# Kernel tuning notes

Hardware: AMD Instinct MI355X
Metric: run time of the kernel (lower is better)

Reference implementation:

```python
import jax, jax.numpy as jnp
import numpy as np

STRIDES = (4, 8, 16, 32, 64)
SIZES = (32.0, 64.0, 128.0, 256.0, 512.0)
ASPECT_RATIOS = np.array([0.5, 1.0, 2.0], dtype=np.float32)
IMG_H = IMG_W = 1024.0
PRE_NMS_TOPK = 1000   # per level (test)
POST_NMS_TOPK = 1000  # per image (test)
NMS_THRESH = 0.7
SCALE_CLAMP = float(np.log(1000.0 / 16.0))
LVL_OFFSET = 4096.0   # > max image coord, for batched (per-level) NMS


def _conv(x, w, b, pad):
    y = jax.lax.conv_general_dilated(x, w, (1, 1), pad,
                                     dimension_numbers=('NCHW', 'OIHW', 'NCHW'))
    return y + b[None, :, None, None]


def _level_anchors(H, W, stride, size):
    # cell anchors: area = size^2, h/w = aspect_ratio
    ar = jnp.asarray(ASPECT_RATIOS)
    w = size / jnp.sqrt(ar)
    h = w * ar
    base = jnp.stack([-w / 2, -h / 2, w / 2, h / 2], axis=1)  # [A,4]
    sx = (jnp.arange(W) * stride).astype(jnp.float32)
    sy = (jnp.arange(H) * stride).astype(jnp.float32)
    yy, xx = jnp.meshgrid(sy, sx, indexing='ij')
    shifts = jnp.stack([xx, yy, xx, yy], axis=-1).reshape(-1, 1, 4)  # [HW,1,4]
    return (shifts + base[None]).reshape(-1, 4)  # [H*W*A, 4]


def _decode_and_clip(deltas, anchors):
    wa = anchors[..., 2] - anchors[..., 0]
    ha = anchors[..., 3] - anchors[..., 1]
    cxa = anchors[..., 0] + 0.5 * wa
    cya = anchors[..., 1] + 0.5 * ha
    dx, dy = deltas[..., 0], deltas[..., 1]
    dw = jnp.minimum(deltas[..., 2], SCALE_CLAMP)
    dh = jnp.minimum(deltas[..., 3], SCALE_CLAMP)
    cx = dx * wa + cxa
    cy = dy * ha + cya
    w = jnp.exp(dw) * wa
    h = jnp.exp(dh) * ha
    x1 = jnp.clip(cx - 0.5 * w, 0.0, IMG_W)
    y1 = jnp.clip(cy - 0.5 * h, 0.0, IMG_H)
    x2 = jnp.clip(cx + 0.5 * w, 0.0, IMG_W)
    y2 = jnp.clip(cy + 0.5 * h, 0.0, IMG_H)
    return jnp.stack([x1, y1, x2, y2], axis=-1)


def _nms_single(raw_boxes, off_boxes, scores):
    # greedy NMS on (level-offset) boxes; returns POST_NMS_TOPK boxes + scores
    N = scores.shape[0]
    order = jnp.argsort(-scores)
    b = jax.lax.stop_gradient(off_boxes[order])
    rb = raw_boxes[order]
    s = scores[order]
    areas = (b[:, 2] - b[:, 0]) * (b[:, 3] - b[:, 1])
    idxs = jnp.arange(N)

    def body(i, sup):
        lt = jnp.maximum(b[i, :2], b[:, :2])
        rbr = jnp.minimum(b[i, 2:], b[:, 2:])
        wh = jnp.clip(rbr - lt, 0.0)
        inter = wh[:, 0] * wh[:, 1]
        iou = inter / (areas[i] + areas - inter + 1e-9)
        return sup | ((~sup[i]) & (iou > NMS_THRESH) & (idxs > i))

    sup = jax.lax.fori_loop(0, N, body, jnp.zeros((N,), bool))
    masked = jnp.where(sup, -1e9, s)
    top_s, top_i = jax.lax.top_k(masked, POST_NMS_TOPK)
    return rb[top_i], top_s


def _rpn_forward(feats, conv_w, conv_b, obj_w, obj_b, delta_w, delta_b):
    all_boxes, all_off, all_scores = [], [], []
    for lvl, (x, stride, size) in enumerate(zip(feats, STRIDES, SIZES)):
        t = jax.nn.relu(_conv(x, conv_w, conv_b, ((1, 1), (1, 1))))
        obj = _conv(t, obj_w, obj_b, ((0, 0), (0, 0)))        # [B,A,H,W]
        dlt = _conv(t, delta_w, delta_b, ((0, 0), (0, 0)))    # [B,4A,H,W]
        B, A, H, W = obj.shape
        obj = obj.transpose(0, 2, 3, 1).reshape(B, -1)        # [B, H*W*A]
        dlt = dlt.reshape(B, A, 4, H, W).transpose(0, 3, 4, 1, 2).reshape(B, -1, 4)
        anchors = _level_anchors(H, W, stride, size)          # [H*W*A, 4]
        k = min(PRE_NMS_TOPK, H * W * A)
        scores_k, idx = jax.lax.top_k(obj, k)                 # [B,k]
        deltas_k = jnp.take_along_axis(dlt, idx[..., None], axis=1)
        anchors_k = anchors[idx]                              # [B,k,4]
        boxes = _decode_and_clip(deltas_k, anchors_k)         # [B,k,4]
        all_boxes.append(boxes)
        all_off.append(boxes + lvl * LVL_OFFSET)              # per-level NMS trick
        all_scores.append(scores_k)
    boxes = jnp.concatenate(all_boxes, axis=1)    # [B, M, 4]
    off = jnp.concatenate(all_off, axis=1)        # [B, M, 4]
    scores = jnp.concatenate(all_scores, axis=1)  # [B, M]
    prop, sc = jax.vmap(_nms_single)(boxes, off, scores)  # [B,K,4], [B,K]
    return jnp.concatenate([prop, sc[..., None]], axis=-1)  # [B,K,5]


def setup_inputs() -> dict:
    key = jax.random.key(0)
    ks = jax.random.split(key, 10)
    C = 256
    shapes = [(2, C, 256, 256), (2, C, 128, 128), (2, C, 64, 64), (2, C, 32, 32), (2, C, 16, 16)]
    inp = {}
    for i, sh in enumerate(shapes):
        inp[f'feat{i}'] = jax.random.normal(ks[i], sh, dtype=jnp.float32)
    inp['conv_w'] = jax.random.normal(ks[5], (C, C, 3, 3), dtype=jnp.float32) * 0.02
    inp['conv_b'] = jnp.zeros((C,), jnp.float32)
    inp['obj_w'] = jax.random.normal(ks[6], (3, C, 1, 1), dtype=jnp.float32) * 0.02
    inp['obj_b'] = jnp.zeros((3,), jnp.float32)
    inp['delta_w'] = jax.random.normal(ks[7], (12, C, 1, 1), dtype=jnp.float32) * 0.02
    inp['delta_b'] = jnp.zeros((12,), jnp.float32)
    return inp


def reference(feat0, feat1, feat2, feat3, feat4, conv_w, conv_b, obj_w, obj_b, delta_w, delta_b):
    feats = [feat0, feat1, feat2, feat3, feat4]
    return _rpn_forward(feats, conv_w, conv_b, obj_w, obj_b, delta_w, delta_b)
```

## Files before the change

kernel.cpp:

```cpp
#include <hip/hip_runtime.h>
#include <cstdint>

#define PIX_TOTAL 87296
#define ATOT      261888
#define PS        2618880
#define MTOT      4768
#define SCALE_CLAMP 4.135166556742356f
#define WSTR      65

__device__ __forceinline__ unsigned fmono(float f) {
  unsigned u = __float_as_uint(f);
  return (u & 0x80000000u) ? ~u : (u | 0x80000000u);
}
__device__ __forceinline__ int lvl_pxb(int l) {
  switch (l) { case 0: return 0; case 1: return 65536; case 2: return 81920;
               case 3: return 86016; default: return 87040; }
}

template<int TW, int TH, int PXT>
__global__ void __launch_bounds__(512, 4)
conv3_fused(const float* __restrict__ feat, const float* __restrict__ cw,
            const float* __restrict__ cbias, const float* __restrict__ ow,
            const float* __restrict__ dw, float* __restrict__ partial,
            int H, int W, int px_base)
{
  constexpr int SR    = TW + 4;
  constexpr int ROWSZ = (TH + 2) * SR;
  constexpr int IN_N  = 8 * ROWSZ;
  constexpr int NR    = PXT / 4 + 1;

  const int tid  = threadIdx.x;
  const int tc   = tid & 7;
  const int tp   = tid >> 3;
  const int cblk = blockIdx.y;
  const int img  = blockIdx.z;
  const int tilesx = W / TW;
  const int ty = blockIdx.x / tilesx;
  const int tx = blockIdx.x - ty * tilesx;
  const int y0 = ty * TH, x0 = tx * TW;
  const int p  = tp * PXT;
  const int py = p / TW, px = p % TW;

  __shared__ __align__(16) float in_lds[IN_N];
  __shared__ __align__(16) float w_lds[8 * 9 * WSTR];
  __shared__ __align__(16) float wo_lds[15 * 64];

  for (int l = tid; l < 960; l += 512) {
    int o = l >> 6, c = l & 63;
    int cg = cblk * 64 + c;
    wo_lds[l] = (o < 3) ? ow[o * 256 + cg] : dw[(o - 3) * 256 + cg];
  }

  float acc[PXT][8];
  #pragma unroll
  for (int j = 0; j < PXT; ++j)
    #pragma unroll
    for (int c = 0; c < 8; ++c) acc[j][c] = 0.f;

  const float* fbase = feat + (size_t)img * 256 * H * W;

  for (int c0 = 0; c0 < 256; c0 += 8) {
    __syncthreads();
    for (int l = tid; l < IN_N; l += 512) {
      int ci  = l / ROWSZ;
      int rem = l - ci * ROWSZ;
      int yy  = rem / SR, xx = rem - yy * SR;
      int gy = y0 - 1 + yy, gx = x0 - 1 + xx;
      float v = 0.f;
      if (gy >= 0 && gy < H && gx >= 0 && gx < W)
        v = fbase[((c0 + ci) * H + gy) * W + gx];
      in_lds[l] = v;
    }
    {
      int oc = tid >> 3, ci = tid & 7;
      const float* wp = cw + ((size_t)(cblk * 64 + oc) * 256 + (c0 + ci)) * 9;
      #pragma unroll
      for (int tap = 0; tap < 9; ++tap)
        w_lds[(ci * 9 + tap) * WSTR + oc] = wp[tap];
    }
    __syncthreads();
    for (int ci = 0; ci < 8; ++ci) {
      #pragma unroll
      for (int ky = 0; ky < 3; ++ky) {
        const float* row = &in_lds[(ci * (TH + 2) + py + ky) * SR + px];
        float win[4 * NR];
        #pragma unroll
        for (int rr = 0; rr < NR; ++rr) {
          float4 rv = *(const float4*)(row + 4 * rr);
          win[4*rr+0] = rv.x; win[4*rr+1] = rv.y;
          win[4*rr+2] = rv.z; win[4*rr+3] = rv.w;
        }
        #pragma unroll
        for (int kx = 0; kx < 3; ++kx) {
          const float* wb = &w_lds[(ci * 9 + ky * 3 + kx) * WSTR + tc * 8];
          float4 w0 = *(const float4*)wb;
          float4 w1 = *(const float4*)(wb + 4);
          #pragma unroll
          for (int j = 0; j < PXT; ++j) {
            float bv = win[j + kx];
            acc[j][0] = fmaf(bv, w0.x, acc[j][0]);
            acc[j][1] = fmaf(bv, w0.y, acc[j][1]);
            acc[j][2] = fmaf(bv, w0.z, acc[j][2]);
            acc[j][3] = fmaf(bv, w0.w, acc[j][3]);
            acc[j][4] = fmaf(bv, w1.x, acc[j][4]);
            acc[j][5] = fmaf(bv, w1.y, acc[j][5]);
            acc[j][6] = fmaf(bv, w1.z, acc[j][6]);
            acc[j][7] = fmaf(bv, w1.w, acc[j][7]);
          }
        }
      }
    }
  }

  float tv[PXT][8];
  #pragma unroll
  for (int c = 0; c < 8; ++c) {
    float b = cbias[cblk * 64 + tc * 8 + c];
    #pragma unroll
    for (int j = 0; j < PXT; ++j) tv[j][c] = fmaxf(acc[j][c] + b, 0.f);
  }
  const int gy = y0 + py;
  const int gx0 = x0 + px;
  const size_t pbase = (size_t)cblk * PS +
      ((size_t)img * PIX_TOTAL + px_base + gy * W + gx0) * 15;
  for (int o = 0; o < 15; ++o) {
    const float* wb = &wo_lds[o * 64 + tc * 8];
    float4 w0 = *(const float4*)wb;
    float4 w1 = *(const float4*)(wb + 4);
    float s[PXT];
    #pragma unroll
    for (int j = 0; j < PXT; ++j)
      s[j] = tv[j][0]*w0.x + tv[j][1]*w0.y + tv[j][2]*w0.z + tv[j][3]*w0.w
           + tv[j][4]*w1.x + tv[j][5]*w1.y + tv[j][6]*w1.z + tv[j][7]*w1.w;
    #pragma unroll
    for (int m = 1; m < 8; m <<= 1) {
      #pragma unroll
      for (int j = 0; j < PXT; ++j) s[j] += __shfl_xor(s[j], m, 64);
    }
    if (tc == 0) {
      #pragma unroll
      for (int j = 0; j < PXT; ++j)
        partial[pbase + (size_t)j * 15 + o] = s[j];
    }
  }
}

__global__ void __launch_bounds__(256)
reduce_kernel(const float* __restrict__ partial, const float* __restrict__ ob,
              const float* __restrict__ db, float* __restrict__ scores,
              float* __restrict__ deltas)
{
  int v = blockIdx.x * 256 + threadIdx.x;
  if (v >= PS) return;
  float s = ((partial[v] + partial[(size_t)PS + v]) + partial[(size_t)2 * PS + v])
            + partial[(size_t)3 * PS + v];
  int o = v % 15;
  int pv = v / 15;
  if (o < 3) {
    scores[(size_t)pv * 3 + o] = s + ob[o];
  } else {
    int c = o - 3;
    deltas[((size_t)pv * 3 + (c >> 2)) * 4 + (c & 3)] = s + db[c];
  }
}

__global__ void __launch_bounds__(1024)
topk_kernel(const float* __restrict__ scores, float* __restrict__ sel_s,
            unsigned* __restrict__ sel_i)
{
  const int tid = threadIdx.x;
  const int bid = blockIdx.x;
  const int img = bid / 5, lvl = bid % 5;
  const int W = 256 >> lvl;
  const int N = W * W * 3;
  const int k = N < 1000 ? N : 1000;
  const float* sc = scores + (size_t)img * ATOT + (size_t)lvl_pxb(lvl) * 3;

  __shared__ unsigned hist[256];
  __shared__ unsigned sh_pref, sh_want;
  __shared__ int cnt_gt, cnt_tie;
  __shared__ float ss[1024];
  __shared__ unsigned si[1024];
  __shared__ unsigned ties[2048];

  unsigned prefix = 0; unsigned want = (unsigned)k;
  for (int pass = 0; pass < 4; ++pass) {
    const int shift = 24 - 8 * pass;
    if (tid < 256) hist[tid] = 0;
    __syncthreads();
    for (int i = tid; i < N; i += 1024) {
      unsigned u = fmono(sc[i]);
      if (pass == 0 || (u >> (shift + 8)) == prefix)
        atomicAdd(&hist[(u >> shift) & 255u], 1u);
    }
    __syncthreads();
    if (tid == 0) {
      unsigned cum = 0; int b = 255;
      for (; b > 0; --b) {
        if (cum + hist[b] >= want) break;
        cum += hist[b];
      }
      sh_pref = (prefix << 8) | (unsigned)b;
      sh_want = want - cum;
    }
    __syncthreads();
    prefix = sh_pref; want = sh_want;
    __syncthreads();
  }
  const unsigned T = prefix;

  ss[tid] = -3e38f; si[tid] = 0xFFFFFFFFu;
  if (tid == 0) { cnt_gt = 0; cnt_tie = 0; }
  __syncthreads();
  for (int i = tid; i < N; i += 1024) {
    float f = sc[i];
    unsigned u = fmono(f);
    if (u > T) {
      int pos = atomicAdd(&cnt_gt, 1);
      ss[pos] = f; si[pos] = (unsigned)i;
    } else if (u == T) {
      int pos = atomicAdd(&cnt_tie, 1);
      if (pos < 2048) ties[pos] = (unsigned)i;
    }
  }
  __syncthreads();
  const int cg = cnt_gt;
  int need = k - cg;
  const int tn = cnt_tie < 2048 ? cnt_tie : 2048;
  if (need > tn) need = tn;
  for (int e = tid; e < tn; e += 1024) {
    unsigned mye = ties[e];
    int rank = 0;
    for (int j = 0; j < tn; ++j) rank += (ties[j] < mye) ? 1 : 0;
    if (rank < need) { ss[cg + rank] = sc[mye]; si[cg + rank] = mye; }
  }
  __syncthreads();
  for (int k2 = 2; k2 <= 1024; k2 <<= 1) {
    for (int j2 = k2 >> 1; j2 > 0; j2 >>= 1) {
      int l2 = tid ^ j2;
      if (l2 > tid) {
        float a = ss[tid], b = ss[l2];
        unsigned ia = si[tid], ib = si[l2];
        bool less = (a < b) || (a == b && ia > ib);
        bool up = ((tid & k2) == 0);
        if (less == up) { ss[tid] = b; ss[l2] = a; si[tid] = ib; si[l2] = ia; }
      }
      __syncthreads();
    }
  }
  sel_s[(size_t)bid * 1024 + tid] = ss[tid];
  sel_i[(size_t)bid * 1024 + tid] = si[tid];
}

__global__ void __launch_bounds__(256)
decode_kernel(const unsigned* __restrict__ sel_i, const float* __restrict__ deltas,
              float* __restrict__ braw, float* __restrict__ boff)
{
  int g = blockIdx.x * 256 + threadIdx.x;
  if (g >= 10240) return;
  int bid = g >> 10, r = g & 1023;
  int img = bid / 5, lvl = bid % 5;
  int W = 256 >> lvl, N = W * W * 3;
  int k = N < 1000 ? N : 1000;
  if (r >= k) return;
  unsigned idx = sel_i[(size_t)bid * 1024 + r];
  float obx[4] = {0.f, 0.f, 0.f, 0.f};
  if (idx < (unsigned)N) {
    int a = idx % 3;
    int pix = idx / 3;
    int x = pix % W, y = pix / W;
    float ar = (a == 0) ? 0.5f : (a == 1 ? 1.0f : 2.0f);
    float sz = (float)(32 << lvl);
    float stridef = (float)(4 << lvl);
    float wa0 = __fdiv_rn(sz, __fsqrt_rn(ar));
    float ha0 = __fmul_rn(wa0, ar);
    float sx = __fmul_rn((float)x, stridef);
    float sy = __fmul_rn((float)y, stridef);
    float x1a = __fadd_rn(sx, -0.5f * wa0);
    float y1a = __fadd_rn(sy, -0.5f * ha0);
    float x2a = __fadd_rn(sx,  0.5f * wa0);
    float y2a = __fadd_rn(sy,  0.5f * ha0);
    float wa  = __fsub_rn(x2a, x1a);
    float ha  = __fsub_rn(y2a, y1a);
    float cxa = __fadd_rn(x1a, __fmul_rn(0.5f, wa));
    float cya = __fadd_rn(y1a, __fmul_rn(0.5f, ha));
    const float* dl = deltas + ((size_t)img * ATOT + (size_t)lvl_pxb(lvl) * 3 + idx) * 4;
    float dx = dl[0], dy = dl[1];
    float dwv = fminf(dl[2], SCALE_CLAMP);
    float dhv = fminf(dl[3], SCALE_CLAMP);
    float cx = __fadd_rn(__fmul_rn(dx, wa), cxa);
    float cy = __fadd_rn(__fmul_rn(dy, ha), cya);
    float wb = __fmul_rn(expf(dwv), wa);
    float hb = __fmul_rn(expf(dhv), ha);
    obx[0] = fminf(fmaxf(__fsub_rn(cx, __fmul_rn(0.5f, wb)), 0.f), 1024.f);
    obx[1] = fminf(fmaxf(__fsub_rn(cy, __fmul_rn(0.5f, hb)), 0.f), 1024.f);
    obx[2] = fminf(fmaxf(__fadd_rn(cx, __fmul_rn(0.5f, wb)), 0.f), 1024.f);
    obx[3] = fminf(fmaxf(__fadd_rn(cy, __fmul_rn(0.5f, hb)), 0.f), 1024.f);
  }
  float loff = (float)lvl * 4096.0f;
  size_t o = ((size_t)bid * 1024 + r) * 4;
  braw[o + 0] = obx[0]; braw[o + 1] = obx[1];
  braw[o + 2] = obx[2]; braw[o + 3] = obx[3];
  boff[o + 0] = __fadd_rn(obx[0], loff); boff[o + 1] = __fadd_rn(obx[1], loff);
  boff[o + 2] = __fadd_rn(obx[2], loff); boff[o + 3] = __fadd_rn(obx[3], loff);
}

__global__ void __launch_bounds__(256)
nms_kernel(const float* __restrict__ boff, unsigned* __restrict__ sup_out)
{
  const int bid = blockIdx.x;
  const int lvl = bid % 5;
  const int W = 256 >> lvl;
  const int N = W * W * 3;
  const int k = N < 1000 ? N : 1000;
  const int tid = threadIdx.x;
  __shared__ float bx1[1000], by1[1000], bx2[1000], by2[1000], bar_[1000];
  __shared__ int sup[1000];
  for (int i = tid; i < k; i += 256) {
    const float* b = boff + ((size_t)bid * 1024 + i) * 4;
    float x1 = b[0], y1 = b[1], x2 = b[2], y2 = b[3];
    bx1[i] = x1; by1[i] = y1; bx2[i] = x2; by2[i] = y2;
    bar_[i] = __fmul_rn(__fsub_rn(x2, x1), __fsub_rn(y2, y1));
    sup[i] = 0;
  }
  __syncthreads();
  for (int i = 0; i < k - 1; ++i) {
    if (!sup[i]) {
      float xi1 = bx1[i], yi1 = by1[i], xi2 = bx2[i], yi2 = by2[i], ai = bar_[i];
      for (int j = i + 1 + tid; j < k; j += 256) {
        if (sup[j]) continue;
        float lx = fmaxf(xi1, bx1[j]);
        float ly = fmaxf(yi1, by1[j]);
        float rx = fminf(xi2, bx2[j]);
        float ry = fminf(yi2, by2[j]);
        float w2 = fmaxf(__fsub_rn(rx, lx), 0.f);
        float h2 = fmaxf(__fsub_rn(ry, ly), 0.f);
        float inter = __fmul_rn(w2, h2);
        float den = __fadd_rn(__fsub_rn(__fadd_rn(ai, bar_[j]), inter), 1e-9f);
        if (__fdiv_rn(inter, den) > 0.7f) sup[j] = 1;
      }
    }
    __syncthreads();
  }
  for (int i = tid; i < k; i += 256) sup_out[(size_t)bid * 1024 + i] = (unsigned)sup[i];
}

__global__ void __launch_bounds__(1024)
merge_kernel(const float* __restrict__ sel_s, const unsigned* __restrict__ sup,
             const float* __restrict__ braw, float* __restrict__ out)
{
  const int img = blockIdx.x;
  const int tid = threadIdx.x;
  __shared__ float ms[MTOT];
  for (int e = tid; e < MTOT; e += 1024) {
    int lvl = e < 4000 ? e / 1000 : 4;
    int r = e - lvl * 1000;
    size_t p2 = (size_t)(img * 5 + lvl) * 1024 + r;
    ms[e] = sup[p2] ? -1e9f : sel_s[p2];
  }
  __syncthreads();
  for (int e = tid; e < MTOT; e += 1024) {
    float me = ms[e];
    int rank = 0;
    for (int j = 0; j < MTOT; ++j) {
      float mj = ms[j];
      rank += (mj > me || (mj == me && j < e)) ? 1 : 0;
    }
    if (rank < 1000) {
      int lvl = e < 4000 ? e / 1000 : 4;
      int r = e - lvl * 1000;
      const float* b = braw + ((size_t)(img * 5 + lvl) * 1024 + r) * 4;
      float* o = out + ((size_t)img * 1000 + rank) * 5;
      o[0] = b[0]; o[1] = b[1]; o[2] = b[2]; o[3] = b[3]; o[4] = me;
    }
  }
}

extern "C" void kernel_launch(void* const* d_in, const int* in_sizes, int n_in,
                              void* d_out, int out_size, void* d_ws, size_t ws_size,
                              hipStream_t stream)
{
  const float* f0 = (const float*)d_in[0];
  const float* f1 = (const float*)d_in[1];
  const float* f2 = (const float*)d_in[2];
  const float* f3 = (const float*)d_in[3];
  const float* f4 = (const float*)d_in[4];
  const float* cw = (const float*)d_in[5];
  const float* cb = (const float*)d_in[6];
  const float* ow = (const float*)d_in[7];
  const float* ob = (const float*)d_in[8];
  const float* dw = (const float*)d_in[9];
  const float* db = (const float*)d_in[10];
  float* out = (float*)d_out;

  float* ws       = (float*)d_ws;
  float* partial  = ws;
  float* scores   = ws + (size_t)4 * PS;
  float* deltas   = scores + (size_t)2 * ATOT;
  float* sel_s    = deltas + (size_t)8 * ATOT;
  unsigned* sel_i = (unsigned*)(sel_s + 10240);
  float* braw     = (float*)(sel_i + 10240);
  float* boff     = braw + 40960;
  unsigned* sup   = (unsigned*)(boff + 40960);

  conv3_fused<128, 4, 8><<<dim3(128, 4, 2), 512, 0, stream>>>(f0, cw, cb, ow, dw, partial, 256, 256, 0);
  conv3_fused<128, 4, 8><<<dim3( 32, 4, 2), 512, 0, stream>>>(f1, cw, cb, ow, dw, partial, 128, 128, 65536);
  conv3_fused< 64, 8, 8><<<dim3(  8, 4, 2), 512, 0, stream>>>(f2, cw, cb, ow, dw, partial,  64,  64, 81920);
  conv3_fused< 32,16, 8><<<dim3(  2, 4, 2), 512, 0, stream>>>(f3, cw, cb, ow, dw, partial,  32,  32, 86016);
  conv3_fused< 16,16, 4><<<dim3(  1, 4, 2), 512, 0, stream>>>(f4, cw, cb, ow, dw, partial,  16,  16, 87040);
  reduce_kernel<<<PS / 256, 256, 0, stream>>>(partial, ob, db, scores, deltas);
  topk_kernel<<<10, 1024, 0, stream>>>(scores, sel_s, sel_i);
  decode_kernel<<<40, 256, 0, stream>>>(sel_i, deltas, braw, boff);
  nms_kernel<<<10, 256, 0, stream>>>(boff, sup);
  merge_kernel<<<2, 1024, 0, stream>>>(sel_s, sup, braw, out);
}
```

Baseline: 9.503 ms.

## Replace serial NMS with bitmask IoU matrix and single-wave suppression scan

Replaces the per-level greedy NMS, which ran one block-wide barrier per candidate box, with two phases. First all pairwise IoU tests are computed in parallel into 64-bit suppression masks held in shared memory. Then a single wavefront scans the rows sequentially using shuffles and no block barriers. It also drops the minBlocks=4 occupancy hint on the conv kernel's launch bounds, which relaxes the register cap. The cost is about 128KB of shared memory for the masks, and every pair is now computed even when the box is already suppressed.

```diff
diff --git a/kernel.cpp b/kernel.cpp
--- a/kernel.cpp
+++ b/kernel.cpp
@@ -7,6 +7,7 @@
 #define MTOT      4768
 #define SCALE_CLAMP 4.135166556742356f
 #define WSTR      65
+#define NW        16
 
 __device__ __forceinline__ unsigned fmono(float f) {
   unsigned u = __float_as_uint(f);
@@ -18,7 +19,7 @@
 }
 
 template<int TW, int TH, int PXT>
-__global__ void __launch_bounds__(512, 4)
+__global__ void __launch_bounds__(512)
 conv3_fused(const float* __restrict__ feat, const float* __restrict__ cw,
             const float* __restrict__ cbias, const float* __restrict__ ow,
             const float* __restrict__ dw, float* __restrict__ partial,
@@ -305,8 +306,9 @@
   boff[o + 2] = __fadd_rn(obx[2], loff); boff[o + 3] = __fadd_rn(obx[3], loff);
 }
 
-__global__ void __launch_bounds__(256)
-nms_kernel(const float* __restrict__ boff, unsigned* __restrict__ sup_out)
+#define BBI(j) ((j) + ((j) >> 6))
+__global__ void __launch_bounds__(1024)
+nms_fused(const float* __restrict__ boff, unsigned* __restrict__ sup_out)
 {
   const int bid = blockIdx.x;
   const int lvl = bid % 5;
@@ -314,35 +316,67 @@
   const int N = W * W * 3;
   const int k = N < 1000 ? N : 1000;
   const int tid = threadIdx.x;
-  __shared__ float bx1[1000], by1[1000], bx2[1000], by2[1000], bar_[1000];
-  __shared__ int sup[1000];
-  for (int i = tid; i < k; i += 256) {
+
+  __shared__ __align__(16) float4 bb[1016];
+  __shared__ float ba[1016];
+  __shared__ unsigned long long masks[1000 * NW];
+  __shared__ unsigned long long supw_sh[NW];
+
+  for (int i = tid; i < k; i += 1024) {
     const float* b = boff + ((size_t)bid * 1024 + i) * 4;
-    float x1 = b[0], y1 = b[1], x2 = b[2], y2 = b[3];
-    bx1[i] = x1; by1[i] = y1; bx2[i] = x2; by2[i] = y2;
-    bar_[i] = __fmul_rn(__fsub_rn(x2, x1), __fsub_rn(y2, y1));
-    sup[i] = 0;
-  }
-  __syncthreads();
-  for (int i = 0; i < k - 1; ++i) {
-    if (!sup[i]) {
-      float xi1 = bx1[i], yi1 = by1[i], xi2 = bx2[i], yi2 = by2[i], ai = bar_[i];
-      for (int j = i + 1 + tid; j < k; j += 256) {
-        if (sup[j]) continue;
-        float lx = fmaxf(xi1, bx1[j]);
-        float ly = fmaxf(yi1, by1[j]);
-        float rx = fminf(xi2, bx2[j]);
-        float ry = fminf(yi2, by2[j]);
+    float4 v = {b[0], b[1], b[2], b[3]};
+    bb[BBI(i)] = v;
+    ba[BBI(i)] = __fmul_rn(__fsub_rn(v.z, v.x), __fsub_rn(v.w, v.y));
+  }
+  __syncthreads();
+
+  for (int t = tid; t < k * NW; t += 1024) {
+    int i = t >> 4;
+    int w = t & 15;
+    unsigned long long m = 0ull;
+    int j0 = w << 6;
+    if (j0 + 63 > i) {
+      float4 vi = bb[BBI(i)];
+      float ai = ba[BBI(i)];
+      int jend = (j0 + 64 < k) ? j0 + 64 : k;
+      int js = (j0 > i + 1) ? j0 : i + 1;
+      for (int j = js; j < jend; ++j) {
+        float4 vj = bb[BBI(j)];
+        float lx = fmaxf(vi.x, vj.x);
+        float ly = fmaxf(vi.y, vj.y);
+        float rx = fminf(vi.z, vj.z);
+        float ry = fminf(vi.w, vj.w);
         float w2 = fmaxf(__fsub_rn(rx, lx), 0.f);
         float h2 = fmaxf(__fsub_rn(ry, ly), 0.f);
         float inter = __fmul_rn(w2, h2);
-        float den = __fadd_rn(__fsub_rn(__fadd_rn(ai, bar_[j]), inter), 1e-9f);
-        if (__fdiv_rn(inter, den) > 0.7f) sup[j] = 1;
+        float den = __fadd_rn(__fsub_rn(__fadd_rn(ai, ba[BBI(j)]), inter), 1e-9f);
+        if (__fdiv_rn(inter, den) > 0.7f) m |= 1ull << (j - j0);
       }
     }
-    __syncthreads();
-  }
-  for (int i = tid; i < k; i += 256) sup_out[(size_t)bid * 1024 + i] = (unsigned)sup[i];
+    masks[t] = m;
+  }
+  __syncthreads();
+
+  if (tid < 64) {
+    const int lane = tid;
+    const int ml = (lane < NW) ? lane : 0;
+    unsigned long long supw = 0ull;
+    unsigned long long mcur = masks[ml];
+    for (int i = 0; i < k; ++i) {
+      int inext = (i + 1 < k) ? i + 1 : i;
+      unsigned long long mnext = masks[inext * NW + ml];
+      int wi = i >> 6;
+      unsigned long long wv = __shfl(supw, wi, 64);
+      if (((wv >> (i & 63)) & 1ull) == 0ull && lane < NW)
+        supw |= mcur;
+      mcur = mnext;
+    }
+    if (lane < NW) supw_sh[lane] = supw;
+  }
+  __syncthreads();
+  for (int i = tid; i < k; i += 1024)
+    sup_out[(size_t)bid * 1024 + i] =
+        (unsigned)((supw_sh[i >> 6] >> (i & 63)) & 1ull);
 }
 
 __global__ void __launch_bounds__(1024)
@@ -411,6 +445,6 @@
   reduce_kernel<<<PS / 256, 256, 0, stream>>>(partial, ob, db, scores, deltas);
   topk_kernel<<<10, 1024, 0, stream>>>(scores, sel_s, sel_i);
   decode_kernel<<<40, 256, 0, stream>>>(sel_i, deltas, braw, boff);
-  nms_kernel<<<10, 256, 0, stream>>>(boff, sup);
+  nms_fused<<<10, 1024, 0, stream>>>(boff, sup);
   merge_kernel<<<2, 1024, 0, stream>>>(sel_s, sup, braw, out);
 }
```

New measurement: 9.275 ms. 1.02x faster.
